# Optimization experiments

Hardware: AMD Instinct MI355X
Metric: run time of the kernel (lower is better)

The kernel has to match this reference:

```python
import jax, jax.numpy as jnp
import numpy as np

B, S, D = 8, 2048, 256
MASK_FILL = -1e9


def setup_inputs() -> dict:
    key = jax.random.key(0)
    kq, kk, kv = jax.random.split(key, 3)
    query = jax.random.normal(kq, (B, S, D), dtype=jnp.float32)
    k_ = jax.random.normal(kk, (B, S, D), dtype=jnp.float32)
    value = jax.random.normal(kv, (B, S, D), dtype=jnp.float32)
    # causal mask: True = masked (gets -1e9), broadcast over batch
    causal = jnp.triu(jnp.ones((S, S), dtype=bool), k=1)
    mask = jnp.broadcast_to(causal, (B, S, S))
    return {"query": query, "key": k_, "value": value, "mask": mask}


def reference(query, key, value, mask):
    d = jnp.asarray(query.shape[-1], dtype=query.dtype)
    # (B,S,S) = bmm(Q, K^T) / sqrt(D)
    attention = jnp.einsum('bqd,bkd->bqk', query, key) / jnp.sqrt(d)
    attention = jnp.where(mask, jnp.asarray(MASK_FILL, attention.dtype), attention)
    attention = jax.nn.softmax(attention, axis=2)
    # dropout p=0.0 -> identity
    out = jnp.einsum('bqk,bkd->bqd', attention, value)
    return out, attention
```

## Files before the change

kernel.cpp:

```cpp
#include <hip/hip_runtime.h>
#include <hip/hip_bf16.h>

typedef __attribute__((ext_vector_type(4))) float  f32x4;
typedef __attribute__((ext_vector_type(8))) __bf16 bf16x8;

constexpr int Bn = 8, Sn = 2048, Dn = 256;
#define SCALE 0.0625f

__device__ float  g_lpart[(size_t)Bn * Sn * 16];
__device__ float  g_linv[(size_t)Bn * Sn];
__device__ __bf16 g_vt[(size_t)Bn * Dn * Sn];
__device__ __bf16 g_praw[(size_t)Bn * Sn * Sn];

__device__ __forceinline__ f32x4 mfma_bf16(bf16x8 a, bf16x8 b, f32x4 c) {
  return __builtin_amdgcn_mfma_f32_16x16x32_bf16(a, b, c, 0, 0, 0);
}

__device__ __forceinline__ bf16x8 cvt8(const float* p) {
  const f32x4* q = (const f32x4*)p;
  f32x4 u0 = q[0], u1 = q[1];
  bf16x8 r;
#pragma unroll
  for (int j = 0; j < 4; ++j) { r[j] = (__bf16)u0[j]; r[4 + j] = (__bf16)u1[j]; }
  return r;
}

__global__ __launch_bounds__(256) void k_vt(const float* __restrict__ V) {
  __shared__ __bf16 t[64][65];
  int bx = blockIdx.x;
  int b = bx >> 7, rem = bx & 127;
  int s0 = (rem >> 2) << 6, d0 = (rem & 3) << 6;
  int tid = threadIdx.x;
#pragma unroll
  for (int i = 0; i < 16; ++i) {
    int idx = tid + (i << 8);
    int r = idx >> 6, c = idx & 63;
    t[r][c] = (__bf16)V[((size_t)(b * Sn + s0 + r) << 8) + d0 + c];
  }
  __syncthreads();
#pragma unroll
  for (int i = 0; i < 16; ++i) {
    int idx = tid + (i << 8);
    int r = idx >> 6, c = idx & 63;
    g_vt[((size_t)(b * Dn + d0 + r) << 11) + s0 + c] = t[c][r];
  }
}

__global__ __launch_bounds__(512) void k_qk(const float* __restrict__ Q,
                                            const float* __restrict__ K) {
  __shared__ __align__(16) char lds[34816];
  __bf16 (*Ab)[64] = reinterpret_cast<__bf16(*)[64]>(lds);
  __bf16 (*Bb)[64] = reinterpret_cast<__bf16(*)[64]>(lds + 16384);
  __bf16 (*pbuf)[136] = reinterpret_cast<__bf16(*)[136]>(lds);
  __shared__ float s_lp[128][4];

  int tid = threadIdx.x;
  int w = tid >> 6, lane = tid & 63, g = lane >> 4, c = lane & 15;
  int mi = w >> 2, ni = w & 3;
  int b = blockIdx.x & 7;
  int idx = blockIdx.x >> 3;
  int mt = 15 - (idx >> 4), nt = idx & 15;
  if (nt > mt) return;

  int grow0 = mt << 7, gcol0 = nt << 7;
  const float* Qb = Q + (size_t)(b * Sn) * Dn;
  const float* Kb = K + (size_t)(b * Sn) * Dn;

  f32x4 acc[4][2];
#pragma unroll
  for (int m2 = 0; m2 < 4; ++m2)
#pragma unroll
    for (int n2 = 0; n2 < 2; ++n2) acc[m2][n2] = {0.f, 0.f, 0.f, 0.f};

  for (int kb = 0; kb < 4; ++kb) {
    int k0 = kb << 6;
    {
      int r = tid >> 2, u0 = (tid & 3) << 1;
      const float* qs = Qb + (size_t)(grow0 + r) * Dn + k0;
      const float* ks = Kb + (size_t)(gcol0 + r) * Dn + k0;
#pragma unroll
      for (int e = 0; e < 2; ++e) {
        int u = u0 + e, su = u ^ (r & 7);
        *reinterpret_cast<bf16x8*>(&Ab[r][su << 3]) = cvt8(qs + (u << 3));
        *reinterpret_cast<bf16x8*>(&Bb[r][su << 3]) = cvt8(ks + (u << 3));
      }
    }
    __syncthreads();
#pragma unroll
    for (int dk = 0; dk < 2; ++dk) {
      bf16x8 af[4], bfr[2];
#pragma unroll
      for (int m2 = 0; m2 < 4; ++m2) {
        int rr = (mi << 6) + (m2 << 4) + c;
        int uu = (g + (dk << 2)) ^ (rr & 7);
        af[m2] = *reinterpret_cast<const bf16x8*>(&Ab[rr][uu << 3]);
      }
#pragma unroll
      for (int n2 = 0; n2 < 2; ++n2) {
        int rr = (ni << 5) + (n2 << 4) + c;
        int uu = (g + (dk << 2)) ^ (rr & 7);
        bfr[n2] = *reinterpret_cast<const bf16x8*>(&Bb[rr][uu << 3]);
      }
#pragma unroll
      for (int m2 = 0; m2 < 4; ++m2)
#pragma unroll
        for (int n2 = 0; n2 < 2; ++n2)
          acc[m2][n2] = mfma_bf16(af[m2], bfr[n2], acc[m2][n2]);
    }
    __syncthreads();
  }

  bool diag = (nt == mt);
#pragma unroll
  for (int m2 = 0; m2 < 4; ++m2) {
#pragma unroll
    for (int r = 0; r < 4; ++r) {
      int row_l = (mi << 6) + (m2 << 4) + (g << 2) + r;
      float lp = 0.f;
#pragma unroll
      for (int n2 = 0; n2 < 2; ++n2) {
        int col_l = (ni << 5) + (n2 << 4) + c;
        float e = (!diag || col_l <= row_l) ? __expf(acc[m2][n2][r] * SCALE) : 0.f;
        pbuf[row_l][col_l] = (__bf16)e;
        lp += e;
      }
#pragma unroll
      for (int off = 1; off < 16; off <<= 1) lp += __shfl_xor(lp, off, 64);
      if (c == 0) s_lp[row_l][ni] = lp;
    }
  }
  __syncthreads();

  {
    int r = tid >> 2, q = tid & 3;
    __bf16* dst =
        g_praw + ((size_t)b << 22) + ((size_t)(grow0 + r) << 11) + gcol0 + (q << 5);
#pragma unroll
    for (int i = 0; i < 4; ++i)
      *reinterpret_cast<bf16x8*>(dst + (i << 3)) =
          *reinterpret_cast<const bf16x8*>(&pbuf[r][(q << 5) + (i << 3)]);
    if (tid < 128) {
      float s = (s_lp[tid][0] + s_lp[tid][1]) + (s_lp[tid][2] + s_lp[tid][3]);
      g_lpart[((size_t)b * Sn + grow0 + tid) * 16 + nt] = s;
    }
  }
}

__global__ __launch_bounds__(256) void k_linv() {
  int i = blockIdx.x * 256 + threadIdx.x;
  const f32x4* p = reinterpret_cast<const f32x4*>(g_lpart + (size_t)i * 16);
  f32x4 s = (p[0] + p[1]) + (p[2] + p[3]);
  g_linv[i] = 1.f / ((s[0] + s[1]) + (s[2] + s[3]));
}

__global__ __launch_bounds__(256, 4) void k_pv(float* __restrict__ P,
                                               float* __restrict__ O) {
  __shared__ __align__(16) __bf16 abuf[32][64];
  __shared__ __align__(16) __bf16 vbuf[128][64];
  int tid = threadIdx.x;
  int w = tid >> 6, lane = tid & 63, g = lane >> 4, c = lane & 15;
  int b = blockIdx.x & 7;
  int idx = blockIdx.x >> 3;
  int dh = idx & 1;
  int mt = 63 - (idx >> 1);
  int row0 = mt << 5;
  int nc = (mt + 2) >> 1;
  const __bf16* prb = g_praw + ((size_t)b << 22);
  const __bf16* vtb = g_vt + ((size_t)(b * Dn + (dh << 7)) << 11);
  float* Pb = P + ((size_t)b << 22);

  int sr = tid >> 3, su = tid & 7;
  const __bf16* sp = prb + ((size_t)(row0 + sr) << 11) + (su << 3);
  float slv = g_linv[(b << 11) + row0 + sr];
  float* spw = Pb + ((size_t)(row0 + sr) << 11) + (su << 3);
  int swu = (su ^ (sr & 7)) << 3;
  const __bf16* vpp = vtb + ((size_t)sr << 11) + (su << 3);

  f32x4 acc[2][2];
#pragma unroll
  for (int m2 = 0; m2 < 2; ++m2)
#pragma unroll
    for (int n2 = 0; n2 < 2; ++n2) acc[m2][n2] = {0.f, 0.f, 0.f, 0.f};

  bf16x8 pr = *reinterpret_cast<const bf16x8*>(sp);
  bf16x8 vt0 = *reinterpret_cast<const bf16x8*>(vpp);
  bf16x8 vt1 = *reinterpret_cast<const bf16x8*>(vpp + (32 << 11));
  bf16x8 vt2 = *reinterpret_cast<const bf16x8*>(vpp + (64 << 11));
  bf16x8 vt3 = *reinterpret_cast<const bf16x8*>(vpp + (96 << 11));

  for (int j = 0; j < nc; ++j) {
    __syncthreads();
    *reinterpret_cast<bf16x8*>(&abuf[sr][swu]) = pr;
    *reinterpret_cast<bf16x8*>(&vbuf[sr][swu]) = vt0;
    *reinterpret_cast<bf16x8*>(&vbuf[sr + 32][swu]) = vt1;
    *reinterpret_cast<bf16x8*>(&vbuf[sr + 64][swu]) = vt2;
    *reinterpret_cast<bf16x8*>(&vbuf[sr + 96][swu]) = vt3;
    if (dh == 0) {
      f32x4 p0, p1;
#pragma unroll
      for (int e = 0; e < 4; ++e) {
        p0[e] = (float)pr[e] * slv;
        p1[e] = (float)pr[4 + e] * slv;
      }
      float* pw = spw + ((size_t)j << 6);
      *reinterpret_cast<f32x4*>(pw) = p0;
      *reinterpret_cast<f32x4*>(pw + 4) = p1;
    }
    __syncthreads();

    if (j + 1 < nc) {
      const __bf16* sp2 = sp + ((size_t)(j + 1) << 6);
      const __bf16* vp2 = vpp + ((size_t)(j + 1) << 6);
      pr = *reinterpret_cast<const bf16x8*>(sp2);
      vt0 = *reinterpret_cast<const bf16x8*>(vp2);
      vt1 = *reinterpret_cast<const bf16x8*>(vp2 + (32 << 11));
      vt2 = *reinterpret_cast<const bf16x8*>(vp2 + (64 << 11));
      vt3 = *reinterpret_cast<const bf16x8*>(vp2 + (96 << 11));
    }

#pragma unroll
    for (int kk = 0; kk < 2; ++kk) {
      bf16x8 a0 = *reinterpret_cast<const bf16x8*>(
          &abuf[c][(((kk << 2) + g) ^ (c & 7)) << 3]);
      bf16x8 a1 = *reinterpret_cast<const bf16x8*>(
          &abuf[16 + c][(((kk << 2) + g) ^ (c & 7)) << 3]);
      int dr0 = (w << 5) + c, dr1 = dr0 + 16;
      bf16x8 b0 = *reinterpret_cast<const bf16x8*>(
          &vbuf[dr0][(((kk << 2) + g) ^ (dr0 & 7)) << 3]);
      bf16x8 b1 = *reinterpret_cast<const bf16x8*>(
          &vbuf[dr1][(((kk << 2) + g) ^ (dr1 & 7)) << 3]);
      acc[0][0] = mfma_bf16(a0, b0, acc[0][0]);
      acc[0][1] = mfma_bf16(a0, b1, acc[0][1]);
      acc[1][0] = mfma_bf16(a1, b0, acc[1][0]);
      acc[1][1] = mfma_bf16(a1, b1, acc[1][1]);
    }
  }

  if (dh == 0) {
    int zc0 = nc << 6;
    float* prow = Pb + ((size_t)(row0 + sr) << 11);
    f32x4 z = {0.f, 0.f, 0.f, 0.f};
    for (int col = zc0 + (su << 2); col < Sn; col += 32)
      *reinterpret_cast<f32x4*>(prow + col) = z;
  }

#pragma unroll
  for (int m2 = 0; m2 < 2; ++m2)
#pragma unroll
    for (int n2 = 0; n2 < 2; ++n2)
#pragma unroll
      for (int r = 0; r < 4; ++r) {
        int row = row0 + (m2 << 4) + (g << 2) + r;
        O[((size_t)(b * Sn + row) << 8) + (dh << 7) + (w << 5) + (n2 << 4) + c] =
            acc[m2][n2][r] * g_linv[(b << 11) + row];
      }
}

extern "C" void kernel_launch(void* const* d_in, const int* in_sizes, int n_in,
                              void* d_out, int out_size, void* d_ws, size_t ws_size,
                              hipStream_t stream) {
  const float* Q = (const float*)d_in[0];
  const float* K = (const float*)d_in[1];
  const float* V = (const float*)d_in[2];

  float* out  = (float*)d_out;
  float* attn = out + (size_t)Bn * Sn * Dn;

  hipLaunchKernelGGL(k_vt, dim3(1024), dim3(256), 0, stream, V);
  hipLaunchKernelGGL(k_qk, dim3(2048), dim3(512), 0, stream, Q, K);
  hipLaunchKernelGGL(k_linv, dim3(64), dim3(256), 0, stream);
  hipLaunchKernelGGL(k_pv, dim3(1024), dim3(256), 0, stream, attn, out);
}
```

Before: 103.1 us.

## Fuse V transpose into QK kernel and compute inverse row sums inside PV

Merges the V-transpose kernel into the QK kernel as an extra 1024 blocks of the same 512-thread launch. It also drops the separate k_linv kernel: each PV block reduces the partial row sums for its own 32 rows into shared memory. This cuts the pipeline from four launches to two and removes the gaps between kernels. In exchange, the transpose blocks now run at 512 threads and share the QK kernel's LDS footprint, and every PV block repeats a small reduction.

```diff
diff --git a/kernel.cpp b/kernel.cpp
--- a/kernel.cpp
+++ b/kernel.cpp
@@ -8,7 +8,6 @@
 #define SCALE 0.0625f
 
 __device__ float  g_lpart[(size_t)Bn * Sn * 16];
-__device__ float  g_linv[(size_t)Bn * Sn];
 __device__ __bf16 g_vt[(size_t)Bn * Dn * Sn];
 __device__ __bf16 g_praw[(size_t)Bn * Sn * Sn];
 
@@ -25,40 +24,43 @@
   return r;
 }
 
-__global__ __launch_bounds__(256) void k_vt(const float* __restrict__ V) {
-  __shared__ __bf16 t[64][65];
+__global__ __launch_bounds__(512) void k_qkvt(const float* __restrict__ Q,
+                                              const float* __restrict__ K,
+                                              const float* __restrict__ V) {
+  __shared__ __align__(16) char lds[34816];
+  __shared__ float s_lp[128][4];
+  int tid = threadIdx.x;
   int bx = blockIdx.x;
-  int b = bx >> 7, rem = bx & 127;
-  int s0 = (rem >> 2) << 6, d0 = (rem & 3) << 6;
-  int tid = threadIdx.x;
-#pragma unroll
-  for (int i = 0; i < 16; ++i) {
-    int idx = tid + (i << 8);
-    int r = idx >> 6, c = idx & 63;
-    t[r][c] = (__bf16)V[((size_t)(b * Sn + s0 + r) << 8) + d0 + c];
-  }
-  __syncthreads();
-#pragma unroll
-  for (int i = 0; i < 16; ++i) {
-    int idx = tid + (i << 8);
-    int r = idx >> 6, c = idx & 63;
-    g_vt[((size_t)(b * Dn + d0 + r) << 11) + s0 + c] = t[c][r];
-  }
-}
-
-__global__ __launch_bounds__(512) void k_qk(const float* __restrict__ Q,
-                                            const float* __restrict__ K) {
-  __shared__ __align__(16) char lds[34816];
+
+  if (bx < 1024) {
+    __bf16 (*t)[65] = reinterpret_cast<__bf16(*)[65]>(lds);
+    int b = bx >> 7, rem = bx & 127;
+    int s0 = (rem >> 2) << 6, d0 = (rem & 3) << 6;
+#pragma unroll
+    for (int i = 0; i < 8; ++i) {
+      int idx = tid + (i << 9);
+      int r = idx >> 6, c = idx & 63;
+      t[r][c] = (__bf16)V[((size_t)(b * Sn + s0 + r) << 8) + d0 + c];
+    }
+    __syncthreads();
+#pragma unroll
+    for (int i = 0; i < 8; ++i) {
+      int idx = tid + (i << 9);
+      int r = idx >> 6, c = idx & 63;
+      g_vt[((size_t)(b * Dn + d0 + r) << 11) + s0 + c] = t[c][r];
+    }
+    return;
+  }
+
   __bf16 (*Ab)[64] = reinterpret_cast<__bf16(*)[64]>(lds);
   __bf16 (*Bb)[64] = reinterpret_cast<__bf16(*)[64]>(lds + 16384);
   __bf16 (*pbuf)[136] = reinterpret_cast<__bf16(*)[136]>(lds);
-  __shared__ float s_lp[128][4];
-
-  int tid = threadIdx.x;
+
   int w = tid >> 6, lane = tid & 63, g = lane >> 4, c = lane & 15;
   int mi = w >> 2, ni = w & 3;
-  int b = blockIdx.x & 7;
-  int idx = blockIdx.x >> 3;
+  int bq = bx - 1024;
+  int b = bq & 7;
+  int idx = bq >> 3;
   int mt = 15 - (idx >> 4), nt = idx & 15;
   if (nt > mt) return;
 
@@ -146,17 +148,11 @@
   }
 }
 
-__global__ __launch_bounds__(256) void k_linv() {
-  int i = blockIdx.x * 256 + threadIdx.x;
-  const f32x4* p = reinterpret_cast<const f32x4*>(g_lpart + (size_t)i * 16);
-  f32x4 s = (p[0] + p[1]) + (p[2] + p[3]);
-  g_linv[i] = 1.f / ((s[0] + s[1]) + (s[2] + s[3]));
-}
-
 __global__ __launch_bounds__(256, 4) void k_pv(float* __restrict__ P,
                                                float* __restrict__ O) {
   __shared__ __align__(16) __bf16 abuf[32][64];
   __shared__ __align__(16) __bf16 vbuf[128][64];
+  __shared__ float linv_s[32];
   int tid = threadIdx.x;
   int w = tid >> 6, lane = tid & 63, g = lane >> 4, c = lane & 15;
   int b = blockIdx.x & 7;
@@ -169,9 +165,15 @@
   const __bf16* vtb = g_vt + ((size_t)(b * Dn + (dh << 7)) << 11);
   float* Pb = P + ((size_t)b << 22);
 
+  if (tid < 32) {
+    const f32x4* p = reinterpret_cast<const f32x4*>(
+        g_lpart + ((size_t)(b << 11) + row0 + tid) * 16);
+    f32x4 s = (p[0] + p[1]) + (p[2] + p[3]);
+    linv_s[tid] = 1.f / ((s[0] + s[1]) + (s[2] + s[3]));
+  }
+
   int sr = tid >> 3, su = tid & 7;
   const __bf16* sp = prb + ((size_t)(row0 + sr) << 11) + (su << 3);
-  float slv = g_linv[(b << 11) + row0 + sr];
   float* spw = Pb + ((size_t)(row0 + sr) << 11) + (su << 3);
   int swu = (su ^ (sr & 7)) << 3;
   const __bf16* vpp = vtb + ((size_t)sr << 11) + (su << 3);
@@ -187,6 +189,9 @@
   bf16x8 vt1 = *reinterpret_cast<const bf16x8*>(vpp + (32 << 11));
   bf16x8 vt2 = *reinterpret_cast<const bf16x8*>(vpp + (64 << 11));
   bf16x8 vt3 = *reinterpret_cast<const bf16x8*>(vpp + (96 << 11));
+
+  __syncthreads();
+  float slv = linv_s[sr];
 
   for (int j = 0; j < nc; ++j) {
     __syncthreads();
@@ -250,9 +255,9 @@
     for (int n2 = 0; n2 < 2; ++n2)
 #pragma unroll
       for (int r = 0; r < 4; ++r) {
-        int row = row0 + (m2 << 4) + (g << 2) + r;
-        O[((size_t)(b * Sn + row) << 8) + (dh << 7) + (w << 5) + (n2 << 4) + c] =
-            acc[m2][n2][r] * g_linv[(b << 11) + row];
+        int rl = (m2 << 4) + (g << 2) + r;
+        O[((size_t)(b * Sn + row0 + rl) << 8) + (dh << 7) + (w << 5) + (n2 << 4) +
+          c] = acc[m2][n2][r] * linv_s[rl];
       }
 }
 
@@ -266,8 +271,6 @@
   float* out  = (float*)d_out;
   float* attn = out + (size_t)Bn * Sn * Dn;
 
-  hipLaunchKernelGGL(k_vt, dim3(1024), dim3(256), 0, stream, V);
-  hipLaunchKernelGGL(k_qk, dim3(2048), dim3(512), 0, stream, Q, K);
-  hipLaunchKernelGGL(k_linv, dim3(64), dim3(256), 0, stream);
+  hipLaunchKernelGGL(k_qkvt, dim3(3072), dim3(512), 0, stream, Q, K, V);
   hipLaunchKernelGGL(k_pv, dim3(1024), dim3(256), 0, stream, attn, out);
 }
```

Measured after the change: 98.24 us. 1.05x faster.
